# Kernel optimization log

Measured on AMD Instinct MI355X. Metric: run time of the kernel, lower is better.

The kernel has to match this reference:

```python
import jax, jax.numpy as jnp
import numpy as np

NL, D, H, DK, L, F, P, NC, PS = 2, 128, 8, 16, 197, 256, 8, 1000, 16
EPS = 1e-5


def _ln(x, w, b):
    m = jnp.mean(x, -1, keepdims=True)
    v = jnp.mean((x - m) ** 2, -1, keepdims=True)
    return (x - m) * jax.lax.rsqrt(v + EPS) * w + b


def _trop_lin(x, W, b):
    # max-plus (tropical) linear: y_o = max_i (x_i + W[o, i]) + b_o
    return jnp.max(x[..., None, :] + W, axis=-1) + b


def _forward(x, patch_w, patch_b, cls_token, pos_embed, bn_gamma, bn_beta, bn_run_max, bn_run_range,
             n1_w, n1_b, n2_w, n2_b, wq, bq, wk, bk, wv, bv, wo, bo, gate_w, gate_b, temp,
             tu_w, tu_b, lf_a, lf_c, lf_gate, cu_w, cu_b, fg_w, fg_b, dn_w, dn_b,
             fn_w, fn_b, head_w, head_b):
    B, C, Hh, Ww = x.shape
    p = PS
    # patchify: [B,C,H,W] -> [B,num_patches,C*p*p]
    xp = x.reshape(B, C, Hh // p, p, Ww // p, p).transpose(0, 2, 4, 1, 3, 5).reshape(B, -1, C * p * p)
    h = xp @ patch_w.T + patch_b
    h = jnp.concatenate([jnp.broadcast_to(cls_token, (B, 1, D)), h], axis=1) + pos_embed
    # TropicalBatchNorm (eval mode, running buffers)
    h = bn_gamma * ((h - bn_run_max) / (bn_run_range + EPS)) + bn_beta
    scale = DK ** -0.5
    for i in range(NL):
        hn = _ln(h, n1_w[i], n1_b[i])
        Q = _trop_lin(hn, wq[i], bq[i]).reshape(B, L, H, DK).transpose(0, 2, 1, 3)
        K = _trop_lin(hn, wk[i], bk[i]).reshape(B, L, H, DK).transpose(0, 2, 1, 3)
        V = (hn @ wv[i].T + bv[i]).reshape(B, L, H, DK).transpose(0, 2, 1, 3)
        cs = jnp.einsum('bhqd,bhkd->bhqk', Q, K) * scale
        # tropical max-plus scores: max_d(Q_q + K_k)  -> [B,H,L,L]
        ts = jnp.max(Q[:, :, :, None, :] + K[:, :, None, :, :], axis=-1) * scale
        g = jax.nn.sigmoid(hn @ gate_w[i].T + gate_b[i]).transpose(0, 2, 1)[..., None]  # [B,H,L,1]
        attn = jax.nn.softmax((g * ts + (1.0 - g) * cs) / temp[i][None, :, None, None], axis=-1)
        out = jnp.einsum('bhqk,bhkd->bhqd', attn, V).transpose(0, 2, 1, 3).reshape(B, L, D)
        h = h + (out @ wo[i].T + bo[i])
        hn2 = _ln(h, n2_w[i], n2_b[i])
        z = _trop_lin(hn2, tu_w[i], tu_b[i])                 # [B,L,F]
        zp = z[:, :, None, :] * lf_a[i] + lf_c[i]            # [B,L,P,F]
        gl = jax.nn.sigmoid(lf_gate[i])
        trop = gl * jnp.max(zp, axis=2) + (1.0 - gl) * jnp.min(zp, axis=2)
        classical = jax.nn.gelu(hn2 @ cu_w[i].T + cu_b[i], approximate=False)
        gf = jax.nn.sigmoid(hn2 @ fg_w[i].T + fg_b[i])
        fused = gf * trop + (1.0 - gf) * classical
        h = h + (fused @ dn_w[i].T + dn_b[i])
    h = _ln(h, fn_w, fn_b)
    return h[:, 0] @ head_w.T + head_b


def setup_inputs() -> dict:
    ks = iter(jax.random.split(jax.random.key(0), 64))
    rn = lambda shape, s=0.02: jax.random.normal(next(ks), shape, jnp.float32) * s
    return dict(
        x=jax.random.normal(next(ks), (4, 3, 224, 224), jnp.float32),
        patch_w=rn((D, 3 * PS * PS)), patch_b=jnp.zeros((D,), jnp.float32),
        cls_token=rn((1, 1, D)), pos_embed=rn((1, L, D)),
        bn_gamma=jnp.ones((D,), jnp.float32), bn_beta=jnp.zeros((D,), jnp.float32),
        bn_run_max=jnp.zeros((D,), jnp.float32), bn_run_range=jnp.ones((D,), jnp.float32),
        n1_w=jnp.ones((NL, D), jnp.float32) + rn((NL, D)), n1_b=rn((NL, D)),
        n2_w=jnp.ones((NL, D), jnp.float32) + rn((NL, D)), n2_b=rn((NL, D)),
        wq=rn((NL, D, D)), bq=rn((NL, D)),
        wk=rn((NL, D, D)), bk=rn((NL, D)),
        wv=rn((NL, D, D)), bv=rn((NL, D)),
        wo=rn((NL, D, D)), bo=rn((NL, D)),
        gate_w=rn((NL, H, D)), gate_b=2.0 + rn((NL, H)),
        temp=1.0 + 0.1 * jax.random.uniform(next(ks), (NL, H), jnp.float32),
        tu_w=rn((NL, F, D)), tu_b=rn((NL, F)),
        lf_a=rn((NL, P, F), 0.5), lf_c=rn((NL, P, F), 0.1), lf_gate=rn((NL, F), 0.5),
        cu_w=rn((NL, F, D)), cu_b=rn((NL, F)),
        fg_w=rn((NL, F, D)), fg_b=2.0 + rn((NL, F)),
        dn_w=rn((NL, D, F)), dn_b=rn((NL, D)),
        fn_w=jnp.ones((D,), jnp.float32) + rn((D,)), fn_b=rn((D,)),
        head_w=rn((NC, D)), head_b=jnp.zeros((NC,), jnp.float32),
    )


def reference(x, patch_w, patch_b, cls_token, pos_embed, bn_gamma, bn_beta, bn_run_max, bn_run_range,
              n1_w, n1_b, n2_w, n2_b, wq, bq, wk, bk, wv, bv, wo, bo, gate_w, gate_b, temp,
              tu_w, tu_b, lf_a, lf_c, lf_gate, cu_w, cu_b, fg_w, fg_b, dn_w, dn_b,
              fn_w, fn_b, head_w, head_b):
    return _forward(x, patch_w, patch_b, cls_token, pos_embed, bn_gamma, bn_beta, bn_run_max, bn_run_range,
                    n1_w, n1_b, n2_w, n2_b, wq, bq, wk, bk, wv, bv, wo, bo, gate_w, gate_b, temp,
                    tu_w, tu_b, lf_a, lf_c, lf_gate, cu_w, cu_b, fg_w, fg_b, dn_w, dn_b,
                    fn_w, fn_b, head_w, head_b)
```

## Files before the change

### kernel.cpp

```cpp
#include <hip/hip_runtime.h>
#include <math.h>

#define EPSF 1e-5f

__device__ __forceinline__ float sigm(float v){ return 1.f/(1.f+__expf(-v)); }

__device__ __forceinline__ unsigned short f2bf(float f){
    unsigned int b = __float_as_uint(f);
    unsigned int r = (b + 0x7fffu + ((b>>16)&1u)) >> 16;
    return (unsigned short)r;
}

struct BF8 { float w0,w1,w2,w3,w4,w5,w6,w7; };
__device__ __forceinline__ BF8 unpk(uint4 U){
    BF8 o;
    o.w0=__uint_as_float(U.x<<16); o.w1=__uint_as_float(U.x&0xffff0000u);
    o.w2=__uint_as_float(U.y<<16); o.w3=__uint_as_float(U.y&0xffff0000u);
    o.w4=__uint_as_float(U.z<<16); o.w5=__uint_as_float(U.z&0xffff0000u);
    o.w6=__uint_as_float(U.w<<16); o.w7=__uint_as_float(U.w&0xffff0000u);
    return o;
}

#define WS_H    0
#define WS_Q    100864
#define WS_K    201728
#define WS_V    302592
#define WS_G    403456
#define WS_AO   409760
#define WS_GWT  510624
#define WS_HDT  512672
#define WS_BF   640672
#define BW_PWT  0
#define BW_WQT  98304
#define BW_WKT  131072
#define BW_WVT  163840
#define BW_WOT  196608
#define BW_TUT  229376
#define BW_CUT  294912
#define BW_FGT  360448
#define BW_DNT  425984

__global__ __launch_bounds__(256) void k_tr(
    const float* __restrict__ pw, const float* __restrict__ wq, const float* __restrict__ wk,
    const float* __restrict__ wv, const float* __restrict__ wo, const float* __restrict__ gw,
    const float* __restrict__ tu, const float* __restrict__ cu, const float* __restrict__ fg,
    const float* __restrict__ dn, const float* __restrict__ hd, float* __restrict__ ws)
{
    __shared__ float tile[32][33];
    int tn = blockIdx.x, t = threadIdx.x;
    unsigned short* wsb = (unsigned short*)(ws + WS_BF);

    if (tn >= 608) {
        for (int i=t;i<2048;i+=256){
            int m=i>>10, rem=i&1023, k=rem>>3, hh=rem&7;
            ws[WS_GWT + m*1024 + k*8 + hh] = gw[m*1024 + hh*128 + k];
        }
        return;
    }

    const float* srcp; long dstoff; int N, K, NR, nt, kt; int isbf = 1;
    if (tn < 96) {
        srcp=pw; dstoff=BW_PWT; N=128; K=768; NR=128; nt=tn/24; kt=tn%24;
    } else if (tn < 224) {
        int i2=tn-96, inst=i2>>4, lt=i2&15, m2=inst>>1;
        srcp = (m2==0)?wq:(m2==1)?wk:(m2==2)?wv:wo;
        srcp += (inst&1)*16384;
        dstoff = BW_WQT + (long)m2*32768 + (inst&1)*16384;
        N=128; K=128; NR=128; nt=lt>>2; kt=lt&3;
    } else if (tn < 416) {
        int i2=tn-224, inst=i2>>5, lt=i2&31, m2=inst>>1;
        srcp = (m2==0)?tu:(m2==1)?cu:fg;
        srcp += (inst&1)*32768;
        dstoff = BW_TUT + (long)m2*65536 + (inst&1)*32768;
        N=256; K=128; NR=256; nt=lt>>2; kt=lt&3;
    } else if (tn < 480) {
        int i2=tn-416, inst=i2>>5, lt=i2&31;
        srcp = dn + inst*32768; dstoff = BW_DNT + (long)inst*32768;
        N=128; K=256; NR=128; nt=lt>>3; kt=lt&7;
    } else {
        int lt=tn-480; srcp=hd; dstoff=WS_HDT; N=1000; K=128; NR=1000; nt=lt>>2; kt=lt&3;
        isbf = 0;
    }

    int n0=nt*32, k0=kt*32;
    int tr=t>>3, tc=(t&7)*4;
    float4 v={0.f,0.f,0.f,0.f};
    if (n0+tr < NR) v = *(const float4*)(srcp + (size_t)(n0+tr)*K + k0 + tc);
    tile[tr][tc]=v.x; tile[tr][tc+1]=v.y; tile[tr][tc+2]=v.z; tile[tr][tc+3]=v.w;
    __syncthreads();
    int kr=t>>3, nc=(t&7)*4;
    float o0=tile[nc][kr], o1=tile[nc+1][kr], o2=tile[nc+2][kr], o3=tile[nc+3][kr];
    if (isbf) {
        int kk = k0+kr, nn = n0+nc;
        unsigned short* dp = wsb + dstoff + ((size_t)(kk>>1)*2*N + (size_t)nn*2 + (kk&1)*4);
        ushort4 u4; u4.x=f2bf(o0); u4.y=f2bf(o1); u4.z=f2bf(o2); u4.w=f2bf(o3);
        *(ushort4*)dp = u4;
    } else {
        float* dp = ws + dstoff + (size_t)(k0+kr)*N + n0 + nc;
        if (n0+nc+3 < NR) {
            float4 o4={o0,o1,o2,o3};
            *(float4*)dp = o4;
        } else {
            if (n0+nc   < NR) dp[0]=o0;
            if (n0+nc+1 < NR) dp[1]=o1;
            if (n0+nc+2 < NR) dp[2]=o2;
            if (n0+nc+3 < NR) dp[3]=o3;
        }
    }
}

__device__ __forceinline__ void ln512(float hv,
    const float* __restrict__ lw, const float* __restrict__ lb,
    float* hnS, float* red, int t)
{
    int r = t >> 7, d = t & 127;
    float s = hv, s2 = hv*hv;
    #pragma unroll
    for (int o=1;o<64;o<<=1){ s += __shfl_xor(s,o); s2 += __shfl_xor(s2,o); }
    int wid = t >> 6;
    if ((t & 63) == 0){ red[wid] = s; red[8+wid] = s2; }
    __syncthreads();
    float S  = red[2*r]   + red[2*r+1];
    float S2 = red[8+2*r] + red[8+2*r+1];
    float mu = S*(1.f/128.f), var = S2*(1.f/128.f)-mu*mu;
    float rr = rsqrtf(var+EPSF);
    hnS[r*128+d] = (hv-mu)*rr*lw[d]+lb[d];
    __syncthreads();
}

__device__ __forceinline__ void qkvT512(const float* hnS, float* pacc, int r0, int t,
    const unsigned short* __restrict__ wqB, const float* __restrict__ bq,
    const unsigned short* __restrict__ wkB, const float* __restrict__ bk,
    const unsigned short* __restrict__ wvB, const float* __restrict__ bv,
    const float* __restrict__ gwT, const float* __restrict__ gb,
    float* __restrict__ Q, float* __restrict__ Kg, float* __restrict__ V,
    float* __restrict__ g)
{
    if (t < 384) {
        int mat = t >> 7, q4i = t & 31, ks = (t >> 5) & 3;
        const unsigned short* wB = (mat==0) ? wqB : (mat==1) ? wkB : wvB;
        const uint4* wp = (const uint4*)wB + q4i;
        int pbase = ks*16;
        float4 acc[4];
        if (mat < 2) {
            #pragma unroll
            for (int r=0;r<4;++r){ acc[r].x=acc[r].y=acc[r].z=acc[r].w=-1e30f; }
            #pragma unroll
            for (int rnd=0;rnd<2;++rnd){
                uint4 wu[8];
                #pragma unroll
                for (int j=0;j<8;++j) wu[j]=wp[(pbase+rnd*8+j)*32];
                #pragma unroll
                for (int j=0;j<8;++j){
                    BF8 W = unpk(wu[j]);
                    int k = (pbase+rnd*8+j)*2;
                    #pragma unroll
                    for (int r=0;r<4;++r){
                        float a0=hnS[r*128+k], a1=hnS[r*128+k+1];
                        acc[r].x=fmaxf(acc[r].x,fmaxf(a0+W.w0,a1+W.w4));
                        acc[r].y=fmaxf(acc[r].y,fmaxf(a0+W.w1,a1+W.w5));
                        acc[r].z=fmaxf(acc[r].z,fmaxf(a0+W.w2,a1+W.w6));
                        acc[r].w=fmaxf(acc[r].w,fmaxf(a0+W.w3,a1+W.w7));
                    }
                }
            }
        } else {
            #pragma unroll
            for (int r=0;r<4;++r){ acc[r].x=acc[r].y=acc[r].z=acc[r].w=0.f; }
            #pragma unroll
            for (int rnd=0;rnd<2;++rnd){
                uint4 wu[8];
                #pragma unroll
                for (int j=0;j<8;++j) wu[j]=wp[(pbase+rnd*8+j)*32];
                #pragma unroll
                for (int j=0;j<8;++j){
                    BF8 W = unpk(wu[j]);
                    int k = (pbase+rnd*8+j)*2;
                    #pragma unroll
                    for (int r=0;r<4;++r){
                        float a0=hnS[r*128+k], a1=hnS[r*128+k+1];
                        acc[r].x=fmaf(a0,W.w0,fmaf(a1,W.w4,acc[r].x));
                        acc[r].y=fmaf(a0,W.w1,fmaf(a1,W.w5,acc[r].y));
                        acc[r].z=fmaf(a0,W.w2,fmaf(a1,W.w6,acc[r].z));
                        acc[r].w=fmaf(a0,W.w3,fmaf(a1,W.w7,acc[r].w));
                    }
                }
            }
        }
        #pragma unroll
        for (int r=0;r<4;++r)
            *(float4*)(pacc + mat*2048 + ks*512 + r*128 + q4i*4) = acc[r];
    } else {
        int u = t & 127, r = u>>5, hh=(u>>2)&7, ks=u&3;
        const float* a = hnS + r*128;
        float acc = 0.f;
        #pragma unroll
        for (int kb=0;kb<2;++kb){
            float wv16[16];
            #pragma unroll
            for (int j=0;j<16;++j) wv16[j]=gwT[(ks*32+kb*16+j)*8+hh];
            #pragma unroll
            for (int j=0;j<16;++j) acc = fmaf(a[ks*32+kb*16+j], wv16[j], acc);
        }
        acc += __shfl_xor(acc,1);
        acc += __shfl_xor(acc,2);
        if (ks==0) g[(r0+r)*8+hh] = sigm(acc + gb[hh]);
    }
    __syncthreads();
    if (t < 384) {
        int mat=t>>7, d=t&127;
        float* dst = (mat==0) ? Q : (mat==1) ? Kg : V;
        const float* bias = (mat==0) ? bq : (mat==1) ? bk : bv;
        #pragma unroll
        for (int r=0;r<4;++r){
            float p0 = pacc[mat*2048 + 0*512 + r*128 + d];
            float p1 = pacc[mat*2048 + 1*512 + r*128 + d];
            float p2 = pacc[mat*2048 + 2*512 + r*128 + d];
            float p3 = pacc[mat*2048 + 3*512 + r*128 + d];
            float s = (mat < 2) ? fmaxf(fmaxf(p0,p1), fmaxf(p2,p3))
                                : (p0 + p1 + p2 + p3);
            dst[(size_t)(r0+r)*128 + d] = s + bias[d];
        }
    }
}

__global__ __launch_bounds__(512, 2) void k_p1(
    const float* __restrict__ x, const unsigned short* __restrict__ pwB,
    const float* __restrict__ pb,
    const float* __restrict__ clsT, const float* __restrict__ pos,
    const float* __restrict__ bng, const float* __restrict__ bnb,
    const float* __restrict__ bnm, const float* __restrict__ bnr,
    const float* __restrict__ n1w, const float* __restrict__ n1b,
    const unsigned short* __restrict__ wqB, const float* __restrict__ bq,
    const unsigned short* __restrict__ wkB, const float* __restrict__ bk,
    const unsigned short* __restrict__ wvB, const float* __restrict__ bv,
    const float* __restrict__ gwT, const float* __restrict__ gb,
    float* __restrict__ h, float* __restrict__ Q, float* __restrict__ Kg,
    float* __restrict__ V, float* __restrict__ g)
{
    __shared__ __align__(16) float xp[4*768];
    __shared__ __align__(16) float pacc[8192];
    __shared__ __align__(16) float hnS[512];
    __shared__ float red[16];
    int t = threadIdx.x, r0 = blockIdx.x * 4;

    #pragma unroll
    for (int r=0;r<4;++r){
        int row=r0+r, b=row/197, l=row-b*197;
        if (l>0){
            int patch=l-1, ph=patch/14, pc=patch-ph*14;
            const float* xb = x + (size_t)b*150528 + ph*3584 + pc*16;
            for (int i=t;i<768;i+=512){
                int c=i>>8, rr=(i>>4)&15, cc=i&15;
                xp[r*768+i] = xb[c*50176 + rr*224 + cc];
            }
        }
    }
    __syncthreads();

    {
        int q4i = t & 31, ks = t >> 5;
        const uint4* wp = (const uint4*)pwB + q4i;
        int pbase = ks*24;
        float4 acc[4];
        #pragma unroll
        for (int r=0;r<4;++r){ acc[r].x=acc[r].y=acc[r].z=acc[r].w=0.f; }
        #pragma unroll
        for (int rnd=0;rnd<3;++rnd){
            uint4 wu[8];
            #pragma unroll
            for (int j=0;j<8;++j) wu[j]=wp[(pbase+rnd*8+j)*32];
            #pragma unroll
            for (int j=0;j<8;++j){
                BF8 W = unpk(wu[j]);
                int k = (pbase+rnd*8+j)*2;
                #pragma unroll
                for (int r=0;r<4;++r){
                    float a0=xp[r*768+k], a1=xp[r*768+k+1];
                    acc[r].x=fmaf(a0,W.w0,fmaf(a1,W.w4,acc[r].x));
                    acc[r].y=fmaf(a0,W.w1,fmaf(a1,W.w5,acc[r].y));
                    acc[r].z=fmaf(a0,W.w2,fmaf(a1,W.w6,acc[r].z));
                    acc[r].w=fmaf(a0,W.w3,fmaf(a1,W.w7,acc[r].w));
                }
            }
        }
        #pragma unroll
        for (int r=0;r<4;++r)
            *(float4*)(pacc + (ks*4+r)*128 + q4i*4) = acc[r];
    }
    __syncthreads();

    float hres;
    {
        int r=t>>7, d=t&127;
        int row=r0+r, l=row%197;
        float s = 0.f;
        #pragma unroll
        for (int k2=0;k2<16;++k2) s += pacc[(k2*4+r)*128+d];
        float v = (l==0) ? clsT[d] : (s + pb[d]);
        v += pos[l*128+d];
        v = bng[d]*((v-bnm[d])/(bnr[d]+EPSF))+bnb[d];
        hres=v;
        h[row*128+d]=v;
    }
    __syncthreads();
    ln512(hres, n1w, n1b, hnS, red, t);
    qkvT512(hnS, pacc, r0, t, wqB,bq,wkB,bk,wvB,bv,gwT,gb, Q,Kg,V,g);
}

__global__ __launch_bounds__(256) void k_attn(
    const float* __restrict__ Qd, const float* __restrict__ Kd,
    const float* __restrict__ Vd, const float* __restrict__ gd,
    const float* __restrict__ tempL, float* __restrict__ ao)
{
    __shared__ __align__(16) float Ks[197*20];
    __shared__ __align__(16) float Vs[197*20];
    int bid = blockIdx.x, t = threadIdx.x;
    int qc = bid % 7, bh = bid / 7, hh = bh & 7, b = bh >> 3;
    size_t base = (size_t)(b*197)*128 + hh*16;

    {
        const float4* ksrc=(const float4*)(Kd+base);
        const float4* vsrc=(const float4*)(Vd+base);
        float4* kdst=(float4*)Ks; float4* vdst=(float4*)Vs;
        for (int idx=t; idx<788; idx+=256){
            int l=idx>>2, jj=idx&3;
            kdst[l*5+jj]=ksrc[l*32+jj];
            vdst[l*5+jj]=vsrc[l*32+jj];
        }
    }
    __syncthreads();

    int q = qc*32 + (t>>3), j8 = t&7;
    if (q >= 197) return;

    float Qr[16];
    {
        const float4* qp=(const float4*)(Qd+base+(size_t)q*128);
        #pragma unroll
        for (int u=0;u<4;++u){
            float4 v=qp[u];
            Qr[4*u]=v.x; Qr[4*u+1]=v.y; Qr[4*u+2]=v.z; Qr[4*u+3]=v.w;
        }
    }
    float gq = gd[(b*197+q)*8+hh];
    float it = 0.25f / tempL[hh];
    float gg = gq*it, cg = (1.f-gq)*it;

    float m=-1e30f, lsum=0.f, o[16];
    #pragma unroll
    for (int j=0;j<16;++j) o[j]=0.f;

    for (int k=j8;k<197;k+=8){
        const float4* kr4=(const float4*)(Ks+k*20);
        float4 kv0=kr4[0], kv1=kr4[1], kv2=kr4[2], kv3=kr4[3];
        float kr[16] = {kv0.x,kv0.y,kv0.z,kv0.w, kv1.x,kv1.y,kv1.z,kv1.w,
                        kv2.x,kv2.y,kv2.z,kv2.w, kv3.x,kv3.y,kv3.z,kv3.w};
        float cs=0.f, ts=-1e30f;
        #pragma unroll
        for (int j=0;j<16;++j){
            cs=fmaf(Qr[j],kr[j],cs);
            ts=fmaxf(ts,Qr[j]+kr[j]);
        }
        float sc=fmaf(gg,ts,cg*cs);
        if (sc>m){
            float c=__expf(m-sc);
            lsum*=c;
            #pragma unroll
            for (int j=0;j<16;++j) o[j]*=c;
            m=sc;
        }
        float p=__expf(sc-m);
        lsum+=p;
        const float4* vr4=(const float4*)(Vs+k*20);
        float4 vv0=vr4[0], vv1=vr4[1], vv2=vr4[2], vv3=vr4[3];
        float vr[16] = {vv0.x,vv0.y,vv0.z,vv0.w, vv1.x,vv1.y,vv1.z,vv1.w,
                        vv2.x,vv2.y,vv2.z,vv2.w, vv3.x,vv3.y,vv3.z,vv3.w};
        #pragma unroll
        for (int j=0;j<16;++j) o[j]=fmaf(p,vr[j],o[j]);
    }

    #pragma unroll
    for (int mask=1;mask<8;mask<<=1){
        float mo=__shfl_xor(m,mask), lo=__shfl_xor(lsum,mask);
        float mn=fmaxf(m,mo);
        float ea=__expf(m-mn), eb=__expf(mo-mn);
        lsum=lsum*ea+lo*eb;
        #pragma unroll
        for (int j=0;j<16;++j){
            float oo=__shfl_xor(o[j],mask);
            o[j]=o[j]*ea+oo*eb;
        }
        m=mn;
    }

    if (j8==0){
        float inv=1.f/lsum;
        float* orow=ao+base+(size_t)q*128;
        #pragma unroll
        for (int j=0;j<16;++j) orow[j]=o[j]*inv;
    }
}

template <int FINAL>
__global__ __launch_bounds__(512, 2) void k_p34(
    const float* __restrict__ ao, float* __restrict__ h,
    const unsigned short* __restrict__ woB, const float* __restrict__ bo,
    const float* __restrict__ n2w, const float* __restrict__ n2b,
    const unsigned short* __restrict__ tuB, const float* __restrict__ tub,
    const float* __restrict__ laA, const float* __restrict__ laC,
    const float* __restrict__ lgG,
    const unsigned short* __restrict__ cuB, const float* __restrict__ cub,
    const unsigned short* __restrict__ fgB, const float* __restrict__ fgb,
    const unsigned short* __restrict__ dnB, const float* __restrict__ dnb,
    const float* __restrict__ nlw, const float* __restrict__ nlb,
    const unsigned short* __restrict__ wqB, const float* __restrict__ bq,
    const unsigned short* __restrict__ wkB, const float* __restrict__ bk,
    const unsigned short* __restrict__ wvB, const float* __restrict__ bv,
    const float* __restrict__ gwT, const float* __restrict__ gb,
    float* __restrict__ Q, float* __restrict__ Kg, float* __restrict__ V,
    float* __restrict__ g,
    const float* __restrict__ hdT, const float* __restrict__ hdb,
    float* __restrict__ out)
{
    __shared__ __align__(16) float aoS[512];
    __shared__ __align__(16) float pacc[8192];
    __shared__ __align__(16) float hnS[512];
    __shared__ __align__(16) float zP[6144];
    __shared__ __align__(16) float fusedS[1024];
    __shared__ float red[16];
    int t = threadIdx.x, r0 = blockIdx.x * 4;
    int q4i=t&31, ks=t>>5;

    aoS[t] = ao[(size_t)r0*128 + t];
    __syncthreads();

    {
        const uint4* wp=(const uint4*)woB + q4i;
        int pbase = ks*4;
        float4 acc[4];
        #pragma unroll
        for (int r=0;r<4;++r){ acc[r].x=acc[r].y=acc[r].z=acc[r].w=0.f; }
        uint4 wu[4];
        #pragma unroll
        for (int j=0;j<4;++j) wu[j]=wp[(pbase+j)*32];
        #pragma unroll
        for (int j=0;j<4;++j){
            BF8 W = unpk(wu[j]);
            int k = (pbase+j)*2;
            #pragma unroll
            for (int r=0;r<4;++r){
                float a0=aoS[r*128+k], a1=aoS[r*128+k+1];
                acc[r].x=fmaf(a0,W.w0,fmaf(a1,W.w4,acc[r].x));
                acc[r].y=fmaf(a0,W.w1,fmaf(a1,W.w5,acc[r].y));
                acc[r].z=fmaf(a0,W.w2,fmaf(a1,W.w6,acc[r].z));
                acc[r].w=fmaf(a0,W.w3,fmaf(a1,W.w7,acc[r].w));
            }
        }
        #pragma unroll
        for (int r=0;r<4;++r)
            *(float4*)(pacc + (ks*4+r)*128 + q4i*4) = acc[r];
    }
    __syncthreads();

    float hres;
    {
        int r=t>>7, d=t&127;
        float s=0.f;
        #pragma unroll
        for (int k2=0;k2<16;++k2) s += pacc[(k2*4+r)*128+d];
        hres = h[(size_t)(r0+r)*128+d] + s + bo[d];
    }
    __syncthreads();
    ln512(hres, n2w, n2b, hnS, red, t);

    {
        int gidx=t>>6, fq=t&63;
        if (gidx < 6) {
            int mat=gidx>>1, ks2=gidx&1;
            const unsigned short* wBm = (mat==0)? tuB : (mat==1)? cuB : fgB;
            const uint4* wp=(const uint4*)wBm + fq;
            int pbase = ks2*32;
            float4 acc[4];
            if (mat==0){
                #pragma unroll
                for (int r=0;r<4;++r){ acc[r].x=acc[r].y=acc[r].z=acc[r].w=-1e30f; }
                #pragma unroll
                for (int rnd=0;rnd<4;++rnd){
                    uint4 wu[8];
                    #pragma unroll
                    for (int j=0;j<8;++j) wu[j]=wp[(pbase+rnd*8+j)*64];
                    #pragma unroll
                    for (int j=0;j<8;++j){
                        BF8 W = unpk(wu[j]);
                        int k = (pbase+rnd*8+j)*2;
                        #pragma unroll
                        for (int r=0;r<4;++r){
                            float a0=hnS[r*128+k], a1=hnS[r*128+k+1];
                            acc[r].x=fmaxf(acc[r].x,fmaxf(a0+W.w0,a1+W.w4));
                            acc[r].y=fmaxf(acc[r].y,fmaxf(a0+W.w1,a1+W.w5));
                            acc[r].z=fmaxf(acc[r].z,fmaxf(a0+W.w2,a1+W.w6));
                            acc[r].w=fmaxf(acc[r].w,fmaxf(a0+W.w3,a1+W.w7));
                        }
                    }
                }
            } else {
                #pragma unroll
                for (int r=0;r<4;++r){ acc[r].x=acc[r].y=acc[r].z=acc[r].w=0.f; }
                #pragma unroll
                for (int rnd=0;rnd<4;++rnd){
                    uint4 wu[8];
                    #pragma unroll
                    for (int j=0;j<8;++j) wu[j]=wp[(pbase+rnd*8+j)*64];
                    #pragma unroll
                    for (int j=0;j<8;++j){
                        BF8 W = unpk(wu[j]);
                        int k = (pbase+rnd*8+j)*2;
                        #pragma unroll
                        for (int r=0;r<4;++r){
                            float a0=hnS[r*128+k], a1=hnS[r*128+k+1];
                            acc[r].x=fmaf(a0,W.w0,fmaf(a1,W.w4,acc[r].x));
                            acc[r].y=fmaf(a0,W.w1,fmaf(a1,W.w5,acc[r].y));
                            acc[r].z=fmaf(a0,W.w2,fmaf(a1,W.w6,acc[r].z));
                            acc[r].w=fmaf(a0,W.w3,fmaf(a1,W.w7,acc[r].w));
                        }
                    }
                }
            }
            #pragma unroll
            for (int r=0;r<4;++r)
                *(float4*)(zP + mat*2048 + ks2*1024 + r*256 + fq*4) = acc[r];
        }
    }
    __syncthreads();

    #pragma unroll
    for (int s2=0;s2<2;++s2){
        int slot = t + s2*512;
        int r = slot>>8, f = slot&255;
        float z  = fmaxf(zP[r*256+f],        zP[1024+r*256+f]) + tub[f];
        float xc = zP[2048+r*256+f] + zP[3072+r*256+f] + cub[f];
        float gv = zP[4096+r*256+f] + zP[5120+r*256+f] + fgb[f];
        float gl = sigm(lgG[f]);
        float mx=-1e30f, mn=1e30f;
        #pragma unroll
        for (int p=0;p<8;++p){
            float zp=fmaf(z, laA[p*256+f], laC[p*256+f]);
            mx=fmaxf(mx,zp); mn=fminf(mn,zp);
        }
        float trop=gl*mx+(1.f-gl)*mn;
        float cla=0.5f*xc*(1.f+erff(xc*0.70710678118654752f));
        float gf=sigm(gv);
        fusedS[r*256+f]=gf*trop+(1.f-gf)*cla;
    }
    __syncthreads();

    {
        const uint4* wp=(const uint4*)dnB + q4i;
        int pbase = ks*8;
        float4 acc[4];
        #pragma unroll
        for (int r=0;r<4;++r){ acc[r].x=acc[r].y=acc[r].z=acc[r].w=0.f; }
        uint4 wu[8];
        #pragma unroll
        for (int j=0;j<8;++j) wu[j]=wp[(pbase+j)*32];
        #pragma unroll
        for (int j=0;j<8;++j){
            BF8 W = unpk(wu[j]);
            int k = (pbase+j)*2;
            #pragma unroll
            for (int r=0;r<4;++r){
                float a0=fusedS[r*256+k], a1=fusedS[r*256+k+1];
                acc[r].x=fmaf(a0,W.w0,fmaf(a1,W.w4,acc[r].x));
                acc[r].y=fmaf(a0,W.w1,fmaf(a1,W.w5,acc[r].y));
                acc[r].z=fmaf(a0,W.w2,fmaf(a1,W.w6,acc[r].z));
                acc[r].w=fmaf(a0,W.w3,fmaf(a1,W.w7,acc[r].w));
            }
        }
        __syncthreads();
        #pragma unroll
        for (int r=0;r<4;++r)
            *(float4*)(pacc + (ks*4+r)*128 + q4i*4) = acc[r];
    }
    __syncthreads();
    {
        int r=t>>7, d=t&127;
        float s=0.f;
        #pragma unroll
        for (int k2=0;k2<16;++k2) s += pacc[(k2*4+r)*128+d];
        hres += s + dnb[d];
        if (!FINAL) h[(size_t)(r0+r)*128+d]=hres;
    }
    __syncthreads();
    ln512(hres, nlw, nlb, hnS, red, t);

    if (!FINAL) {
        qkvT512(hnS, pacc, r0, t, wqB,bq,wkB,bk,wvB,bv,gwT,gb, Q,Kg,V,g);
    } else {
        int crow=-1, cb2=0;
        #pragma unroll
        for (int r=0;r<4;++r){
            int row=r0+r;
            if (row==0 || row==197 || row==394 || row==591){ crow=r; cb2=row/197; }
        }
        if (crow>=0 && t<500){
            const float2* w2=(const float2*)hdT + t;
            const float* a = hnS + crow*128;
            float acc0=hdb[2*t], acc1=hdb[2*t+1];
            #pragma unroll
            for (int kb=0;kb<16;++kb){
                float2 wv8[8];
                #pragma unroll
                for (int j=0;j<8;++j) wv8[j]=w2[(kb*8+j)*500];
                #pragma unroll
                for (int j=0;j<8;++j){
                    float av=a[kb*8+j];
                    acc0=fmaf(av,wv8[j].x,acc0); acc1=fmaf(av,wv8[j].y,acc1);
                }
            }
            out[cb2*1000+2*t]=acc0;
            out[cb2*1000+2*t+1]=acc1;
        }
    }
}

extern "C" void kernel_launch(void* const* d_in, const int* in_sizes, int n_in,
                              void* d_out, int out_size, void* d_ws, size_t ws_size,
                              hipStream_t stream)
{
    const float* x        = (const float*)d_in[0];
    const float* patch_w  = (const float*)d_in[1];
    const float* patch_b  = (const float*)d_in[2];
    const float* cls_tok  = (const float*)d_in[3];
    const float* pos_emb  = (const float*)d_in[4];
    const float* bn_gamma = (const float*)d_in[5];
    const float* bn_beta  = (const float*)d_in[6];
    const float* bn_rmax  = (const float*)d_in[7];
    const float* bn_rrng  = (const float*)d_in[8];
    const float* n1_w     = (const float*)d_in[9];
    const float* n1_b     = (const float*)d_in[10];
    const float* n2_w     = (const float*)d_in[11];
    const float* n2_b     = (const float*)d_in[12];
    const float* wq       = (const float*)d_in[13];
    const float* bq       = (const float*)d_in[14];
    const float* wk       = (const float*)d_in[15];
    const float* bk       = (const float*)d_in[16];
    const float* wv       = (const float*)d_in[17];
    const float* bv       = (const float*)d_in[18];
    const float* wo       = (const float*)d_in[19];
    const float* bo       = (const float*)d_in[20];
    const float* gate_w   = (const float*)d_in[21];
    const float* gate_b   = (const float*)d_in[22];
    const float* temp     = (const float*)d_in[23];
    const float* tu_w     = (const float*)d_in[24];
    const float* tu_b     = (const float*)d_in[25];
    const float* lf_a     = (const float*)d_in[26];
    const float* lf_c     = (const float*)d_in[27];
    const float* lf_gate  = (const float*)d_in[28];
    const float* cu_w     = (const float*)d_in[29];
    const float* cu_b     = (const float*)d_in[30];
    const float* fg_w     = (const float*)d_in[31];
    const float* fg_b     = (const float*)d_in[32];
    const float* dn_w     = (const float*)d_in[33];
    const float* dn_b     = (const float*)d_in[34];
    const float* fn_w     = (const float*)d_in[35];
    const float* fn_b     = (const float*)d_in[36];
    const float* head_w   = (const float*)d_in[37];
    const float* head_b   = (const float*)d_in[38];

    float* ws = (float*)d_ws;
    float* h   = ws + WS_H;
    float* Q   = ws + WS_Q;
    float* Kb  = ws + WS_K;
    float* V   = ws + WS_V;
    float* g   = ws + WS_G;
    float* ao  = ws + WS_AO;
    unsigned short* wsb = (unsigned short*)(ws + WS_BF);
    float* out = (float*)d_out;

    k_tr<<<609, 256, 0, stream>>>(patch_w, wq, wk, wv, wo, gate_w,
                                  tu_w, cu_w, fg_w, dn_w, head_w, ws);

    k_p1<<<197, 512, 0, stream>>>(x, wsb+BW_PWT, patch_b, cls_tok, pos_emb,
                                  bn_gamma, bn_beta, bn_rmax, bn_rrng,
                                  n1_w, n1_b,
                                  wsb+BW_WQT, bq, wsb+BW_WKT, bk, wsb+BW_WVT, bv,
                                  ws+WS_GWT, gate_b,
                                  h, Q, Kb, V, g);

    k_attn<<<224, 256, 0, stream>>>(Q, Kb, V, g, temp, ao);

    k_p34<0><<<197, 512, 0, stream>>>(ao, h,
        wsb+BW_WOT, bo, n2_w, n2_b,
        wsb+BW_TUT, tu_b, lf_a, lf_c, lf_gate,
        wsb+BW_CUT, cu_b, wsb+BW_FGT, fg_b, wsb+BW_DNT, dn_b,
        n1_w + 128, n1_b + 128,
        wsb+BW_WQT+16384, bq + 128, wsb+BW_WKT+16384, bk + 128,
        wsb+BW_WVT+16384, bv + 128, ws+WS_GWT+1024, gate_b + 8,
        Q, Kb, V, g, nullptr, nullptr, nullptr);

    k_attn<<<224, 256, 0, stream>>>(Q, Kb, V, g, temp + 8, ao);

    k_p34<1><<<197, 512, 0, stream>>>(ao, h,
        wsb+BW_WOT+16384, bo + 128, n2_w + 128, n2_b + 128,
        wsb+BW_TUT+32768, tu_b + 256, lf_a + 2048, lf_c + 2048, lf_gate + 256,
        wsb+BW_CUT+32768, cu_b + 256, wsb+BW_FGT+32768, fg_b + 256,
        wsb+BW_DNT+32768, dn_b + 128,
        fn_w, fn_b,
        nullptr, nullptr, nullptr, nullptr, nullptr, nullptr,
        ws+WS_GWT, gate_b,
        Q, Kb, V, g, ws+WS_HDT, head_b, out);
}
```

Baseline: 77.37 us.

## Process two rows per block with 256 threads to double grid size

The row-wise kernels (patch embed + QKV, and the post-attention MLP/QKV kernel) now handle 2 token rows per 256-thread block instead of 4 rows per 512-thread block, launching 394 blocks instead of 197. The per-thread K-split work partitioning is reshaped: fewer K-splits and longer reduction loops per thread, smaller shared-memory partial buffers, and the tropical/linear up-projections no longer split K across thread groups. The goal is to spread 788 rows over more blocks so all CUs of the device are occupied, at the cost of each block re-reading the full weight matrices for half as many rows. The classifier head is also vectorised to float4 loads over 250 threads.

```diff
diff --git a/kernel.cpp b/kernel.cpp
--- a/kernel.cpp
+++ b/kernel.cpp
@@ -109,7 +109,7 @@
     }
 }
 
-__device__ __forceinline__ void ln512(float hv,
+__device__ __forceinline__ void ln2x(float hv,
     const float* __restrict__ lw, const float* __restrict__ lb,
     float* hnS, float* red, int t)
 {
@@ -117,18 +117,17 @@
     float s = hv, s2 = hv*hv;
     #pragma unroll
     for (int o=1;o<64;o<<=1){ s += __shfl_xor(s,o); s2 += __shfl_xor(s2,o); }
-    int wid = t >> 6;
-    if ((t & 63) == 0){ red[wid] = s; red[8+wid] = s2; }
+    if ((t & 63) == 0){ int wid=t>>6; red[wid]=s; red[4+wid]=s2; }
     __syncthreads();
     float S  = red[2*r]   + red[2*r+1];
-    float S2 = red[8+2*r] + red[8+2*r+1];
+    float S2 = red[4+2*r] + red[4+2*r+1];
     float mu = S*(1.f/128.f), var = S2*(1.f/128.f)-mu*mu;
     float rr = rsqrtf(var+EPSF);
     hnS[r*128+d] = (hv-mu)*rr*lw[d]+lb[d];
     __syncthreads();
 }
 
-__device__ __forceinline__ void qkvT512(const float* hnS, float* pacc, int r0, int t,
+__device__ __forceinline__ void qkv256(const float* hnS, float* pacc, int r0, int t,
     const unsigned short* __restrict__ wqB, const float* __restrict__ bq,
     const unsigned short* __restrict__ wkB, const float* __restrict__ bk,
     const unsigned short* __restrict__ wvB, const float* __restrict__ bv,
@@ -136,26 +135,25 @@
     float* __restrict__ Q, float* __restrict__ Kg, float* __restrict__ V,
     float* __restrict__ g)
 {
-    if (t < 384) {
-        int mat = t >> 7, q4i = t & 31, ks = (t >> 5) & 3;
+    if (t < 192) {
+        int mat = t / 64, u = t & 63, q4i = u & 31, ks = u >> 5;
         const unsigned short* wB = (mat==0) ? wqB : (mat==1) ? wkB : wvB;
         const uint4* wp = (const uint4*)wB + q4i;
-        int pbase = ks*16;
-        float4 acc[4];
+        float4 acc[2];
         if (mat < 2) {
             #pragma unroll
-            for (int r=0;r<4;++r){ acc[r].x=acc[r].y=acc[r].z=acc[r].w=-1e30f; }
-            #pragma unroll
-            for (int rnd=0;rnd<2;++rnd){
+            for (int r=0;r<2;++r){ acc[r].x=acc[r].y=acc[r].z=acc[r].w=-1e30f; }
+            #pragma unroll
+            for (int rnd=0;rnd<4;++rnd){
                 uint4 wu[8];
                 #pragma unroll
-                for (int j=0;j<8;++j) wu[j]=wp[(pbase+rnd*8+j)*32];
+                for (int j=0;j<8;++j) wu[j]=wp[(ks*32+rnd*8+j)*32];
                 #pragma unroll
                 for (int j=0;j<8;++j){
                     BF8 W = unpk(wu[j]);
-                    int k = (pbase+rnd*8+j)*2;
+                    int k = (ks*32+rnd*8+j)*2;
                     #pragma unroll
-                    for (int r=0;r<4;++r){
+                    for (int r=0;r<2;++r){
                         float a0=hnS[r*128+k], a1=hnS[r*128+k+1];
                         acc[r].x=fmaxf(acc[r].x,fmaxf(a0+W.w0,a1+W.w4));
                         acc[r].y=fmaxf(acc[r].y,fmaxf(a0+W.w1,a1+W.w5));
@@ -166,18 +164,18 @@
             }
         } else {
             #pragma unroll
-            for (int r=0;r<4;++r){ acc[r].x=acc[r].y=acc[r].z=acc[r].w=0.f; }
-            #pragma unroll
-            for (int rnd=0;rnd<2;++rnd){
+            for (int r=0;r<2;++r){ acc[r].x=acc[r].y=acc[r].z=acc[r].w=0.f; }
+            #pragma unroll
+            for (int rnd=0;rnd<4;++rnd){
                 uint4 wu[8];
                 #pragma unroll
-                for (int j=0;j<8;++j) wu[j]=wp[(pbase+rnd*8+j)*32];
+                for (int j=0;j<8;++j) wu[j]=wp[(ks*32+rnd*8+j)*32];
                 #pragma unroll
                 for (int j=0;j<8;++j){
                     BF8 W = unpk(wu[j]);
-                    int k = (pbase+rnd*8+j)*2;
+                    int k = (ks*32+rnd*8+j)*2;
                     #pragma unroll
-                    for (int r=0;r<4;++r){
+                    for (int r=0;r<2;++r){
                         float a0=hnS[r*128+k], a1=hnS[r*128+k+1];
                         acc[r].x=fmaf(a0,W.w0,fmaf(a1,W.w4,acc[r].x));
                         acc[r].y=fmaf(a0,W.w1,fmaf(a1,W.w5,acc[r].y));
@@ -188,10 +186,11 @@
             }
         }
         #pragma unroll
-        for (int r=0;r<4;++r)
-            *(float4*)(pacc + mat*2048 + ks*512 + r*128 + q4i*4) = acc[r];
+        for (int r=0;r<2;++r)
+            *(float4*)(pacc + mat*512 + ks*256 + r*128 + q4i*4) = acc[r];
     } else {
-        int u = t & 127, r = u>>5, hh=(u>>2)&7, ks=u&3;
+        int u = t - 192;
+        int r = u>>5, hh=(u>>2)&7, ks=u&3;
         const float* a = hnS + r*128;
         float acc = 0.f;
         #pragma unroll
@@ -207,24 +206,21 @@
         if (ks==0) g[(r0+r)*8+hh] = sigm(acc + gb[hh]);
     }
     __syncthreads();
-    if (t < 384) {
-        int mat=t>>7, d=t&127;
-        float* dst = (mat==0) ? Q : (mat==1) ? Kg : V;
-        const float* bias = (mat==0) ? bq : (mat==1) ? bk : bv;
-        #pragma unroll
-        for (int r=0;r<4;++r){
-            float p0 = pacc[mat*2048 + 0*512 + r*128 + d];
-            float p1 = pacc[mat*2048 + 1*512 + r*128 + d];
-            float p2 = pacc[mat*2048 + 2*512 + r*128 + d];
-            float p3 = pacc[mat*2048 + 3*512 + r*128 + d];
-            float s = (mat < 2) ? fmaxf(fmaxf(p0,p1), fmaxf(p2,p3))
-                                : (p0 + p1 + p2 + p3);
+    {
+        int r=t>>7, d=t&127;
+        #pragma unroll
+        for (int mat=0;mat<3;++mat){
+            float p0 = pacc[mat*512 + 0   + r*128 + d];
+            float p1 = pacc[mat*512 + 256 + r*128 + d];
+            float s = (mat < 2) ? fmaxf(p0,p1) : (p0 + p1);
+            float* dst = (mat==0) ? Q : (mat==1) ? Kg : V;
+            const float* bias = (mat==0) ? bq : (mat==1) ? bk : bv;
             dst[(size_t)(r0+r)*128 + d] = s + bias[d];
         }
     }
 }
 
-__global__ __launch_bounds__(512, 2) void k_p1(
+__global__ __launch_bounds__(256, 2) void k_p1(
     const float* __restrict__ x, const unsigned short* __restrict__ pwB,
     const float* __restrict__ pb,
     const float* __restrict__ clsT, const float* __restrict__ pos,
@@ -238,19 +234,19 @@
     float* __restrict__ h, float* __restrict__ Q, float* __restrict__ Kg,
     float* __restrict__ V, float* __restrict__ g)
 {
-    __shared__ __align__(16) float xp[4*768];
-    __shared__ __align__(16) float pacc[8192];
-    __shared__ __align__(16) float hnS[512];
-    __shared__ float red[16];
-    int t = threadIdx.x, r0 = blockIdx.x * 4;
+    __shared__ __align__(16) float xp[2*768];
+    __shared__ __align__(16) float pacc[2048];
+    __shared__ __align__(16) float hnS[256];
+    __shared__ float red[8];
+    int t = threadIdx.x, r0 = blockIdx.x * 2;
 
     #pragma unroll
-    for (int r=0;r<4;++r){
+    for (int r=0;r<2;++r){
         int row=r0+r, b=row/197, l=row-b*197;
         if (l>0){
             int patch=l-1, ph=patch/14, pc=patch-ph*14;
             const float* xb = x + (size_t)b*150528 + ph*3584 + pc*16;
-            for (int i=t;i<768;i+=512){
+            for (int i=t;i<768;i+=256){
                 int c=i>>8, rr=(i>>4)&15, cc=i&15;
                 xp[r*768+i] = xb[c*50176 + rr*224 + cc];
             }
@@ -261,12 +257,12 @@
     {
         int q4i = t & 31, ks = t >> 5;
         const uint4* wp = (const uint4*)pwB + q4i;
-        int pbase = ks*24;
-        float4 acc[4];
-        #pragma unroll
-        for (int r=0;r<4;++r){ acc[r].x=acc[r].y=acc[r].z=acc[r].w=0.f; }
-        #pragma unroll
-        for (int rnd=0;rnd<3;++rnd){
+        int pbase = ks*48;
+        float4 acc[2];
+        #pragma unroll
+        for (int r=0;r<2;++r){ acc[r].x=acc[r].y=acc[r].z=acc[r].w=0.f; }
+        #pragma unroll
+        for (int rnd=0;rnd<6;++rnd){
             uint4 wu[8];
             #pragma unroll
             for (int j=0;j<8;++j) wu[j]=wp[(pbase+rnd*8+j)*32];
@@ -275,7 +271,7 @@
                 BF8 W = unpk(wu[j]);
                 int k = (pbase+rnd*8+j)*2;
                 #pragma unroll
-                for (int r=0;r<4;++r){
+                for (int r=0;r<2;++r){
                     float a0=xp[r*768+k], a1=xp[r*768+k+1];
                     acc[r].x=fmaf(a0,W.w0,fmaf(a1,W.w4,acc[r].x));
                     acc[r].y=fmaf(a0,W.w1,fmaf(a1,W.w5,acc[r].y));
@@ -285,8 +281,8 @@
             }
         }
         #pragma unroll
-        for (int r=0;r<4;++r)
-            *(float4*)(pacc + (ks*4+r)*128 + q4i*4) = acc[r];
+        for (int r=0;r<2;++r)
+            *(float4*)(pacc + (ks*2+r)*128 + q4i*4) = acc[r];
     }
     __syncthreads();
 
@@ -296,16 +292,16 @@
         int row=r0+r, l=row%197;
         float s = 0.f;
         #pragma unroll
-        for (int k2=0;k2<16;++k2) s += pacc[(k2*4+r)*128+d];
+        for (int k2=0;k2<8;++k2) s += pacc[(k2*2+r)*128+d];
         float v = (l==0) ? clsT[d] : (s + pb[d]);
         v += pos[l*128+d];
         v = bng[d]*((v-bnm[d])/(bnr[d]+EPSF))+bnb[d];
         hres=v;
-        h[row*128+d]=v;
-    }
-    __syncthreads();
-    ln512(hres, n1w, n1b, hnS, red, t);
-    qkvT512(hnS, pacc, r0, t, wqB,bq,wkB,bk,wvB,bv,gwT,gb, Q,Kg,V,g);
+        h[(size_t)row*128+d]=v;
+    }
+    __syncthreads();
+    ln2x(hres, n1w, n1b, hnS, red, t);
+    qkv256(hnS, pacc, r0, t, wqB,bq,wkB,bk,wvB,bv,gwT,gb, Q,Kg,V,g);
 }
 
 __global__ __launch_bounds__(256) void k_attn(
@@ -403,7 +399,7 @@
 }
 
 template <int FINAL>
-__global__ __launch_bounds__(512, 2) void k_p34(
+__global__ __launch_bounds__(256, 2) void k_p34(
     const float* __restrict__ ao, float* __restrict__ h,
     const unsigned short* __restrict__ woB, const float* __restrict__ bo,
     const float* __restrict__ n2w, const float* __restrict__ n2b,
@@ -423,13 +419,13 @@
     const float* __restrict__ hdT, const float* __restrict__ hdb,
     float* __restrict__ out)
 {
-    __shared__ __align__(16) float aoS[512];
-    __shared__ __align__(16) float pacc[8192];
-    __shared__ __align__(16) float hnS[512];
-    __shared__ __align__(16) float zP[6144];
-    __shared__ __align__(16) float fusedS[1024];
-    __shared__ float red[16];
-    int t = threadIdx.x, r0 = blockIdx.x * 4;
+    __shared__ __align__(16) float aoS[256];
+    __shared__ __align__(16) float pacc[2048];
+    __shared__ __align__(16) float hnS[256];
+    __shared__ __align__(16) float zS[1536];
+    __shared__ __align__(16) float fusedS[512];
+    __shared__ float red[8];
+    int t = threadIdx.x, r0 = blockIdx.x * 2;
     int q4i=t&31, ks=t>>5;
 
     aoS[t] = ao[(size_t)r0*128 + t];
@@ -437,19 +433,19 @@
 
     {
         const uint4* wp=(const uint4*)woB + q4i;
-        int pbase = ks*4;
-        float4 acc[4];
-        #pragma unroll
-        for (int r=0;r<4;++r){ acc[r].x=acc[r].y=acc[r].z=acc[r].w=0.f; }
-        uint4 wu[4];
-        #pragma unroll
-        for (int j=0;j<4;++j) wu[j]=wp[(pbase+j)*32];
-        #pragma unroll
-        for (int j=0;j<4;++j){
+        int pbase = ks*8;
+        float4 acc[2];
+        #pragma unroll
+        for (int r=0;r<2;++r){ acc[r].x=acc[r].y=acc[r].z=acc[r].w=0.f; }
+        uint4 wu[8];
+        #pragma unroll
+        for (int j=0;j<8;++j) wu[j]=wp[(pbase+j)*32];
+        #pragma unroll
+        for (int j=0;j<8;++j){
             BF8 W = unpk(wu[j]);
             int k = (pbase+j)*2;
             #pragma unroll
-            for (int r=0;r<4;++r){
+            for (int r=0;r<2;++r){
                 float a0=aoS[r*128+k], a1=aoS[r*128+k+1];
                 acc[r].x=fmaf(a0,W.w0,fmaf(a1,W.w4,acc[r].x));
                 acc[r].y=fmaf(a0,W.w1,fmaf(a1,W.w5,acc[r].y));
@@ -458,8 +454,8 @@
             }
         }
         #pragma unroll
-        for (int r=0;r<4;++r)
-            *(float4*)(pacc + (ks*4+r)*128 + q4i*4) = acc[r];
+        for (int r=0;r<2;++r)
+            *(float4*)(pacc + (ks*2+r)*128 + q4i*4) = acc[r];
     }
     __syncthreads();
 
@@ -468,79 +464,75 @@
         int r=t>>7, d=t&127;
         float s=0.f;
         #pragma unroll
-        for (int k2=0;k2<16;++k2) s += pacc[(k2*4+r)*128+d];
+        for (int k2=0;k2<8;++k2) s += pacc[(k2*2+r)*128+d];
         hres = h[(size_t)(r0+r)*128+d] + s + bo[d];
     }
     __syncthreads();
-    ln512(hres, n2w, n2b, hnS, red, t);
-
-    {
-        int gidx=t>>6, fq=t&63;
-        if (gidx < 6) {
-            int mat=gidx>>1, ks2=gidx&1;
-            const unsigned short* wBm = (mat==0)? tuB : (mat==1)? cuB : fgB;
-            const uint4* wp=(const uint4*)wBm + fq;
-            int pbase = ks2*32;
-            float4 acc[4];
-            if (mat==0){
-                #pragma unroll
-                for (int r=0;r<4;++r){ acc[r].x=acc[r].y=acc[r].z=acc[r].w=-1e30f; }
-                #pragma unroll
-                for (int rnd=0;rnd<4;++rnd){
-                    uint4 wu[8];
+    ln2x(hres, n2w, n2b, hnS, red, t);
+
+    if (t < 192) {
+        int mat = t / 64, fq = t & 63;
+        const unsigned short* wBm = (mat==0)? tuB : (mat==1)? cuB : fgB;
+        const uint4* wp=(const uint4*)wBm + fq;
+        float4 acc[2];
+        if (mat==0){
+            #pragma unroll
+            for (int r=0;r<2;++r){ acc[r].x=acc[r].y=acc[r].z=acc[r].w=-1e30f; }
+            #pragma unroll
+            for (int rnd=0;rnd<8;++rnd){
+                uint4 wu[8];
+                #pragma unroll
+                for (int j=0;j<8;++j) wu[j]=wp[(rnd*8+j)*64];
+                #pragma unroll
+                for (int j=0;j<8;++j){
+                    BF8 W = unpk(wu[j]);
+                    int k = (rnd*8+j)*2;
                     #pragma unroll
-                    for (int j=0;j<8;++j) wu[j]=wp[(pbase+rnd*8+j)*64];
-                    #pragma unroll
-                    for (int j=0;j<8;++j){
-                        BF8 W = unpk(wu[j]);
-                        int k = (pbase+rnd*8+j)*2;
-                        #pragma unroll
-                        for (int r=0;r<4;++r){
-                            float a0=hnS[r*128+k], a1=hnS[r*128+k+1];
-                            acc[r].x=fmaxf(acc[r].x,fmaxf(a0+W.w0,a1+W.w4));
-                            acc[r].y=fmaxf(acc[r].y,fmaxf(a0+W.w1,a1+W.w5));
-                            acc[r].z=fmaxf(acc[r].z,fmaxf(a0+W.w2,a1+W.w6));
-                            acc[r].w=fmaxf(acc[r].w,fmaxf(a0+W.w3,a1+W.w7));
-                        }
+                    for (int r=0;r<2;++r){
+                        float a0=hnS[r*128+k], a1=hnS[r*128+k+1];
+                        acc[r].x=fmaxf(acc[r].x,fmaxf(a0+W.w0,a1+W.w4));
+                        acc[r].y=fmaxf(acc[r].y,fmaxf(a0+W.w1,a1+W.w5));
+                        acc[r].z=fmaxf(acc[r].z,fmaxf(a0+W.w2,a1+W.w6));
+                        acc[r].w=fmaxf(acc[r].w,fmaxf(a0+W.w3,a1+W.w7));
                     }
                 }
-            } else {
-                #pragma unroll
-                for (int r=0;r<4;++r){ acc[r].x=acc[r].y=acc[r].z=acc[r].w=0.f; }
-                #pragma unroll
-                for (int rnd=0;rnd<4;++rnd){
-                    uint4 wu[8];
+            }
+        } else {
+            #pragma unroll
+            for (int r=0;r<2;++r){ acc[r].x=acc[r].y=acc[r].z=acc[r].w=0.f; }
+            #pragma unroll
+            for (int rnd=0;rnd<8;++rnd){
+                uint4 wu[8];
+                #pragma unroll
+                for (int j=0;j<8;++j) wu[j]=wp[(rnd*8+j)*64];
+                #pragma unroll
+                for (int j=0;j<8;++j){
+                    BF8 W = unpk(wu[j]);
+                    int k = (rnd*8+j)*2;
                     #pragma unroll
-                    for (int j=0;j<8;++j) wu[j]=wp[(pbase+rnd*8+j)*64];
-                    #pragma unroll
-                    for (int j=0;j<8;++j){
-                        BF8 W = unpk(wu[j]);
-                        int k = (pbase+rnd*8+j)*2;
-                        #pragma unroll
-                        for (int r=0;r<4;++r){
-                            float a0=hnS[r*128+k], a1=hnS[r*128+k+1];
-                            acc[r].x=fmaf(a0,W.w0,fmaf(a1,W.w4,acc[r].x));
-                            acc[r].y=fmaf(a0,W.w1,fmaf(a1,W.w5,acc[r].y));
-                            acc[r].z=fmaf(a0,W.w2,fmaf(a1,W.w6,acc[r].z));
-                            acc[r].w=fmaf(a0,W.w3,fmaf(a1,W.w7,acc[r].w));
-                        }
+                    for (int r=0;r<2;++r){
+                        float a0=hnS[r*128+k], a1=hnS[r*128+k+1];
+                        acc[r].x=fmaf(a0,W.w0,fmaf(a1,W.w4,acc[r].x));
+                        acc[r].y=fmaf(a0,W.w1,fmaf(a1,W.w5,acc[r].y));
+                        acc[r].z=fmaf(a0,W.w2,fmaf(a1,W.w6,acc[r].z));
+                        acc[r].w=fmaf(a0,W.w3,fmaf(a1,W.w7,acc[r].w));
                     }
                 }
             }
-            #pragma unroll
-            for (int r=0;r<4;++r)
-                *(float4*)(zP + mat*2048 + ks2*1024 + r*256 + fq*4) = acc[r];
-        }
+        }
+        #pragma unroll
+        for (int r=0;r<2;++r)
+            *(float4*)(zS + mat*512 + r*256 + fq*4) = acc[r];
     }
     __syncthreads();
 
     #pragma unroll
     for (int s2=0;s2<2;++s2){
-        int slot = t + s2*512;
+        int slot = t + s2*256;
         int r = slot>>8, f = slot&255;
-        float z  = fmaxf(zP[r*256+f],        zP[1024+r*256+f]) + tub[f];
-        float xc = zP[2048+r*256+f] + zP[3072+r*256+f] + cub[f];
-        float gv = zP[4096+r*256+f] + zP[5120+r*256+f] + fgb[f];
+        float z  = zS[r*256+f]        + tub[f];
+        float xc = zS[512+r*256+f]    + cub[f];
+        float gv = zS[1024+r*256+f]   + fgb[f];
         float gl = sigm(lgG[f]);
         float mx=-1e30f, mn=1e30f;
         #pragma unroll
@@ -557,69 +549,73 @@
 
     {
         const uint4* wp=(const uint4*)dnB + q4i;
-        int pbase = ks*8;
-        float4 acc[4];
-        #pragma unroll
-        for (int r=0;r<4;++r){ acc[r].x=acc[r].y=acc[r].z=acc[r].w=0.f; }
-        uint4 wu[8];
-        #pragma unroll
-        for (int j=0;j<8;++j) wu[j]=wp[(pbase+j)*32];
-        #pragma unroll
-        for (int j=0;j<8;++j){
-            BF8 W = unpk(wu[j]);
-            int k = (pbase+j)*2;
-            #pragma unroll
-            for (int r=0;r<4;++r){
-                float a0=fusedS[r*256+k], a1=fusedS[r*256+k+1];
-                acc[r].x=fmaf(a0,W.w0,fmaf(a1,W.w4,acc[r].x));
-                acc[r].y=fmaf(a0,W.w1,fmaf(a1,W.w5,acc[r].y));
-                acc[r].z=fmaf(a0,W.w2,fmaf(a1,W.w6,acc[r].z));
-                acc[r].w=fmaf(a0,W.w3,fmaf(a1,W.w7,acc[r].w));
+        int pbase = ks*16;
+        float4 acc[2];
+        #pragma unroll
+        for (int r=0;r<2;++r){ acc[r].x=acc[r].y=acc[r].z=acc[r].w=0.f; }
+        #pragma unroll
+        for (int rnd=0;rnd<2;++rnd){
+            uint4 wu[8];
+            #pragma unroll
+            for (int j=0;j<8;++j) wu[j]=wp[(pbase+rnd*8+j)*32];
+            #pragma unroll
+            for (int j=0;j<8;++j){
+                BF8 W = unpk(wu[j]);
+                int k = (pbase+rnd*8+j)*2;
+                #pragma unroll
+                for (int r=0;r<2;++r){
+                    float a0=fusedS[r*256+k], a1=fusedS[r*256+k+1];
+                    acc[r].x=fmaf(a0,W.w0,fmaf(a1,W.w4,acc[r].x));
+                    acc[r].y=fmaf(a0,W.w1,fmaf(a1,W.w5,acc[r].y));
+                    acc[r].z=fmaf(a0,W.w2,fmaf(a1,W.w6,acc[r].z));
+                    acc[r].w=fmaf(a0,W.w3,fmaf(a1,W.w7,acc[r].w));
+                }
             }
         }
         __syncthreads();
         #pragma unroll
-        for (int r=0;r<4;++r)
-            *(float4*)(pacc + (ks*4+r)*128 + q4i*4) = acc[r];
+        for (int r=0;r<2;++r)
+            *(float4*)(pacc + (ks*2+r)*128 + q4i*4) = acc[r];
     }
     __syncthreads();
     {
         int r=t>>7, d=t&127;
         float s=0.f;
         #pragma unroll
-        for (int k2=0;k2<16;++k2) s += pacc[(k2*4+r)*128+d];
+        for (int k2=0;k2<8;++k2) s += pacc[(k2*2+r)*128+d];
         hres += s + dnb[d];
         if (!FINAL) h[(size_t)(r0+r)*128+d]=hres;
     }
     __syncthreads();
-    ln512(hres, nlw, nlb, hnS, red, t);
+    ln2x(hres, nlw, nlb, hnS, red, t);
 
     if (!FINAL) {
-        qkvT512(hnS, pacc, r0, t, wqB,bq,wkB,bk,wvB,bv,gwT,gb, Q,Kg,V,g);
+        qkv256(hnS, pacc, r0, t, wqB,bq,wkB,bk,wvB,bv,gwT,gb, Q,Kg,V,g);
     } else {
         int crow=-1, cb2=0;
         #pragma unroll
-        for (int r=0;r<4;++r){
+        for (int r=0;r<2;++r){
             int row=r0+r;
             if (row==0 || row==197 || row==394 || row==591){ crow=r; cb2=row/197; }
         }
-        if (crow>=0 && t<500){
-            const float2* w2=(const float2*)hdT + t;
+        if (crow>=0 && t<250){
             const float* a = hnS + crow*128;
-            float acc0=hdb[2*t], acc1=hdb[2*t+1];
+            int n0 = 4*t;
+            float4 acc; acc.x=hdb[n0]; acc.y=hdb[n0+1]; acc.z=hdb[n0+2]; acc.w=hdb[n0+3];
             #pragma unroll
             for (int kb=0;kb<16;++kb){
-                float2 wv8[8];
-                #pragma unroll
-                for (int j=0;j<8;++j) wv8[j]=w2[(kb*8+j)*500];
+                float4 wv4[8];
+                #pragma unroll
+                for (int j=0;j<8;++j) wv4[j]=*(const float4*)(hdT + (size_t)(kb*8+j)*1000 + n0);
                 #pragma unroll
                 for (int j=0;j<8;++j){
                     float av=a[kb*8+j];
-                    acc0=fmaf(av,wv8[j].x,acc0); acc1=fmaf(av,wv8[j].y,acc1);
+                    acc.x=fmaf(av,wv4[j].x,acc.x); acc.y=fmaf(av,wv4[j].y,acc.y);
+                    acc.z=fmaf(av,wv4[j].z,acc.z); acc.w=fmaf(av,wv4[j].w,acc.w);
                 }
             }
-            out[cb2*1000+2*t]=acc0;
-            out[cb2*1000+2*t+1]=acc1;
+            out[cb2*1000+n0]=acc.x; out[cb2*1000+n0+1]=acc.y;
+            out[cb2*1000+n0+2]=acc.z; out[cb2*1000+n0+3]=acc.w;
         }
     }
 }
@@ -681,7 +677,7 @@
     k_tr<<<609, 256, 0, stream>>>(patch_w, wq, wk, wv, wo, gate_w,
                                   tu_w, cu_w, fg_w, dn_w, head_w, ws);
 
-    k_p1<<<197, 512, 0, stream>>>(x, wsb+BW_PWT, patch_b, cls_tok, pos_emb,
+    k_p1<<<394, 256, 0, stream>>>(x, wsb+BW_PWT, patch_b, cls_tok, pos_emb,
                                   bn_gamma, bn_beta, bn_rmax, bn_rrng,
                                   n1_w, n1_b,
                                   wsb+BW_WQT, bq, wsb+BW_WKT, bk, wsb+BW_WVT, bv,
@@ -690,7 +686,7 @@
 
     k_attn<<<224, 256, 0, stream>>>(Q, Kb, V, g, temp, ao);
 
-    k_p34<0><<<197, 512, 0, stream>>>(ao, h,
+    k_p34<0><<<394, 256, 0, stream>>>(ao, h,
         wsb+BW_WOT, bo, n2_w, n2_b,
         wsb+BW_TUT, tu_b, lf_a, lf_c, lf_gate,
         wsb+BW_CUT, cu_b, wsb+BW_FGT, fg_b, wsb+BW_DNT, dn_b,
@@ -701,7 +697,7 @@
 
     k_attn<<<224, 256, 0, stream>>>(Q, Kb, V, g, temp + 8, ao);
 
-    k_p34<1><<<197, 512, 0, stream>>>(ao, h,
+    k_p34<1><<<394, 256, 0, stream>>>(ao, h,
         wsb+BW_WOT+16384, bo + 128, n2_w + 128, n2_b + 128,
         wsb+BW_TUT+32768, tu_b + 256, lf_a + 2048, lf_c + 2048, lf_gate + 256,
         wsb+BW_CUT+32768, cu_b + 256, wsb+BW_FGT+32768, fg_b + 256,
```

New measurement: 79.19 us. 1.02x slower.
